# Optimization experiments

Measured on AMD Instinct MI355X. Metric: run time of the kernel, lower is better.

Reference implementation:

```python
import jax, jax.numpy as jnp
import numpy as np

B, T, I, H, O = 8192, 1024, 7, 100, 1


def setup_inputs() -> dict:
    key = jax.random.key(0)
    ks = jax.random.split(key, 7)
    s = 1.0 / np.sqrt(H)  # PyTorch default init bound for RNN/Linear(H)
    return {
        "x": jax.random.normal(ks[0], (B, T, I), dtype=jnp.float32),
        "W_ih": jax.random.uniform(ks[1], (H, I), jnp.float32, -s, s),
        "W_hh": jax.random.uniform(ks[2], (H, H), jnp.float32, -s, s),
        "b_ih": jax.random.uniform(ks[3], (H,), jnp.float32, -s, s),
        "b_hh": jax.random.uniform(ks[4], (H,), jnp.float32, -s, s),
        "W_fc": jax.random.uniform(ks[5], (O, H), jnp.float32, -s, s),
        "b_fc": jax.random.uniform(ks[6], (O,), jnp.float32, -s, s),
    }


def reference(x, W_ih, W_hh, b_ih, b_hh, W_fc, b_fc):
    # Precompute the input projection for all timesteps in one GEMM:
    # x_proj[b,t,h] = x[b,t,:] @ W_ih^T + b_ih + b_hh  (both biases folded in)
    x_proj = jnp.einsum('bti,hi->bth', x, W_ih) + b_ih + b_hh  # [B,T,H]

    def step(h, xt):
        # h_t = relu(x_t W_ih^T + b_ih + h_{t-1} W_hh^T + b_hh)
        h_new = jax.nn.relu(xt + h @ W_hh.T)
        return h_new, None

    h0 = jnp.zeros((x.shape[0], W_hh.shape[0]), dtype=x.dtype)  # [B,H]
    hT, _ = jax.lax.scan(step, h0, jnp.swapaxes(x_proj, 0, 1))  # scan over T

    # fc applied to last timestep only: out[:, -1, :] @ W_fc^T + b_fc
    return hT @ W_fc.T + b_fc  # [B,O]
```

## Files before the change

### kernel.cpp

```cpp
#include <hip/hip_runtime.h>


typedef _Float16 half8 __attribute__((ext_vector_type(8)));
typedef float f32x4 __attribute__((ext_vector_type(4)));
typedef unsigned u32x4 __attribute__((ext_vector_type(4)));

static __device__ __forceinline__ unsigned pkrtz(float a, float b) {
    return __builtin_bit_cast(unsigned, __builtin_amdgcn_cvt_pkrtz(a, b));
}

__global__ __launch_bounds__(64, 1)
void rnn_wave(const float* __restrict__ x,
              const float* __restrict__ W_ih,
              const float* __restrict__ W_hh,
              const float* __restrict__ b_ih,
              const float* __restrict__ b_hh,
              const float* __restrict__ W_fc,
              const float* __restrict__ b_fc,
              float* __restrict__ out) {
    const int l  = threadIdx.x;
    const int lm = l & 15;
    const int q  = l >> 4;
    const bool q1   = (q == 1);
    const bool qlt2 = (q < 2);

    half8 w[7][4];
#pragma unroll
    for (int ti = 0; ti < 7; ++ti) {
        const int np = 16 * ti + lm;
#pragma unroll
        for (int kt = 0; kt < 4; ++kt) {
            half8 hw;
#pragma unroll
            for (int jj = 0; jj < 8; ++jj) {
                float v = 0.f;
                if (np < 100) {
                    if (jj < 4) {
                        int p = 16 * kt + 4 * q + jj;
                        if (p < 100) v = W_hh[np * 100 + p];
                    } else if (kt < 3) {
                        int p = 16 * (kt + 4) + 4 * q + (jj - 4);
                        if (p < 100) v = W_hh[np * 100 + p];
                    } else {
                        if (q == 0)      v = W_ih[np * 7 + (jj - 4)];
                        else if (q == 1) v = (jj < 7) ? W_ih[np * 7 + jj]
                                             : (b_ih[np] + b_hh[np]);
                    }
                }
                hw[jj] = (_Float16)v;
            }
            w[ti][kt] = hw;
        }
    }

    const float* xr = x + (size_t)(blockIdx.x * 16 + lm) * 7168;
    const int o0 = q1 ? 4 : 0, o1 = o0 + 1, o2 = o0 + 2, o3 = q1 ? 6 : 3;

    half8 hf[4];
    {
        float v0 = xr[o0], v1 = xr[o1], v2 = xr[o2], v3 = xr[o3];
        u32x4 z = {0u, 0u, 0u, 0u};
        hf[0] = __builtin_bit_cast(half8, z);
        hf[1] = hf[0];
        hf[2] = hf[0];
        unsigned xd0 = pkrtz(v0, v1);
        unsigned xd1 = pkrtz(v2, q1 ? 1.0f : v3);
        if (!qlt2) { xd0 = 0u; xd1 = 0u; }
        u32x4 h3 = {0u, 0u, xd0, xd1};
        hf[3] = __builtin_bit_cast(half8, h3);
    }

    float xv[4][4];
#pragma unroll
    for (int s = 1; s <= 4; ++s) {
        const float* p = xr + s * 7;
        xv[s & 3][0] = p[o0]; xv[s & 3][1] = p[o1];
        xv[s & 3][2] = p[o2]; xv[s & 3][3] = p[o3];
    }

    const f32x4 kZ = {0.f, 0.f, 0.f, 0.f};
    f32x4 acc[7];

    for (int tb = 0; tb < 1024; tb += 4) {
#pragma unroll
        for (int u = 0; u < 4; ++u) {
            const int t = tb + u;

#pragma unroll
            for (int kt = 0; kt < 4; ++kt) {
                const int order[7] = {0, 4, 1, 5, 2, 6, 3};
#pragma unroll
                for (int oi = 0; oi < 7; ++oi) {
                    const int ti = order[oi];
                    acc[ti] = __builtin_amdgcn_mfma_f32_16x16x32_f16(
                        w[ti][kt], hf[kt], (kt == 0) ? kZ : acc[ti], 0, 0, 0);
                }
            }

            const int s = (u + 1) & 3;
#pragma unroll
            for (int kt = 0; kt < 3; ++kt) {
                u32x4 d;
                d.x = pkrtz(fmaxf(acc[kt][0], 0.f),     fmaxf(acc[kt][1], 0.f));
                d.y = pkrtz(fmaxf(acc[kt][2], 0.f),     fmaxf(acc[kt][3], 0.f));
                d.z = pkrtz(fmaxf(acc[kt + 4][0], 0.f), fmaxf(acc[kt + 4][1], 0.f));
                d.w = pkrtz(fmaxf(acc[kt + 4][2], 0.f), fmaxf(acc[kt + 4][3], 0.f));
                hf[kt] = __builtin_bit_cast(half8, d);
            }
            {
                unsigned xd0 = pkrtz(xv[s][0], xv[s][1]);
                unsigned xd1 = pkrtz(xv[s][2], q1 ? 1.0f : xv[s][3]);
                if (!qlt2) { xd0 = 0u; xd1 = 0u; }
                u32x4 d;
                d.x = pkrtz(fmaxf(acc[3][0], 0.f), fmaxf(acc[3][1], 0.f));
                d.y = pkrtz(fmaxf(acc[3][2], 0.f), fmaxf(acc[3][3], 0.f));
                d.z = xd0; d.w = xd1;
                hf[3] = __builtin_bit_cast(half8, d);
            }

            int tn = t + 5; if (tn > 1023) tn = 1023;
            const float* p = xr + tn * 7;
            xv[s][0] = p[o0]; xv[s][1] = p[o1];
            xv[s][2] = p[o2]; xv[s][3] = p[o3];
        }
    }

    float sum = 0.f;
#pragma unroll
    for (int ti = 0; ti < 7; ++ti) {
#pragma unroll
        for (int r = 0; r < 4; ++r) {
            const int np = 16 * ti + 4 * q + r;
            const float wf = (np < 100) ? W_fc[np] : 0.f;
            sum += wf * fmaxf(acc[ti][r], 0.f);
        }
    }
    sum += __shfl_xor(sum, 16, 64);
    sum += __shfl_xor(sum, 32, 64);
    if (q == 0) out[blockIdx.x * 16 + lm] = sum + b_fc[0];
}

extern "C" void kernel_launch(void* const* d_in, const int* in_sizes, int n_in,
                              void* d_out, int out_size, void* d_ws, size_t ws_size,
                              hipStream_t stream) {
    const float* x    = (const float*)d_in[0];
    const float* W_ih = (const float*)d_in[1];
    const float* W_hh = (const float*)d_in[2];
    const float* b_ih = (const float*)d_in[3];
    const float* b_hh = (const float*)d_in[4];
    const float* W_fc = (const float*)d_in[5];
    const float* b_fc = (const float*)d_in[6];
    float* out = (float*)d_out;

    rnn_wave<<<dim3(512), dim3(64), 0, stream>>>(x, W_ih, W_hh, b_ih, b_hh, W_fc, b_fc, out);
}
```

Baseline: 619.2 us.

## Interleave two independent batch tiles per wave to hide MFMA dependency latency

Each wave now processes two 16-row batch tiles (A and B) in lockstep, with interleaved MFMA chains sharing the same register-resident weights. The grid is halved to 256 blocks. This aims to fill the MFMA pipeline with independent work, since a single tile's serial recurrence leaves it stalled on dependency latency. ReLU is applied as a packed half max after conversion rather than as an fp32 fmaxf, and x loads are predicated to the lanes that need them. The trade-off is fewer waves across the CUs, on a device that has more CUs than the old 512 blocks, plus higher register pressure.

```diff
diff --git a/kernel.cpp b/kernel.cpp
--- a/kernel.cpp
+++ b/kernel.cpp
@@ -53,33 +53,43 @@
         }
     }
 
-    const float* xr = x + (size_t)(blockIdx.x * 16 + lm) * 7168;
+    const float* xrA = x + (size_t)(blockIdx.x * 32 + lm) * 7168;
+    const float* xrB = xrA + (size_t)16 * 7168;
     const int o0 = q1 ? 4 : 0, o1 = o0 + 1, o2 = o0 + 2, o3 = q1 ? 6 : 3;
 
-    half8 hf[4];
+    const u32x4 zz = {0u, 0u, 0u, 0u};
+    const half8 hz = __builtin_bit_cast(half8, zz);
+
+    half8 hfA[4], hfB[4];
     {
-        float v0 = xr[o0], v1 = xr[o1], v2 = xr[o2], v3 = xr[o3];
-        u32x4 z = {0u, 0u, 0u, 0u};
-        hf[0] = __builtin_bit_cast(half8, z);
-        hf[1] = hf[0];
-        hf[2] = hf[0];
-        unsigned xd0 = pkrtz(v0, v1);
-        unsigned xd1 = pkrtz(v2, q1 ? 1.0f : v3);
-        if (!qlt2) { xd0 = 0u; xd1 = 0u; }
-        u32x4 h3 = {0u, 0u, xd0, xd1};
-        hf[3] = __builtin_bit_cast(half8, h3);
+        float a0 = xrA[o0], a1 = xrA[o1], a2 = xrA[o2], a3 = xrA[o3];
+        float c0 = xrB[o0], c1 = xrB[o1], c2 = xrB[o2], c3 = xrB[o3];
+        hfA[0] = hz; hfA[1] = hz; hfA[2] = hz;
+        hfB[0] = hz; hfB[1] = hz; hfB[2] = hz;
+        unsigned ad0 = pkrtz(a0, a1), ad1 = pkrtz(a2, q1 ? 1.0f : a3);
+        unsigned bd0 = pkrtz(c0, c1), bd1 = pkrtz(c2, q1 ? 1.0f : c3);
+        if (!qlt2) { ad0 = 0u; ad1 = 0u; bd0 = 0u; bd1 = 0u; }
+        u32x4 ha = {0u, 0u, ad0, ad1};
+        u32x4 hb = {0u, 0u, bd0, bd1};
+        hfA[3] = __builtin_bit_cast(half8, ha);
+        hfB[3] = __builtin_bit_cast(half8, hb);
     }
 
-    float xv[4][4];
+    float xvA[4][4], xvB[4][4];
+    if (qlt2) {
 #pragma unroll
-    for (int s = 1; s <= 4; ++s) {
-        const float* p = xr + s * 7;
-        xv[s & 3][0] = p[o0]; xv[s & 3][1] = p[o1];
-        xv[s & 3][2] = p[o2]; xv[s & 3][3] = p[o3];
+        for (int s = 1; s <= 4; ++s) {
+            const float* pA = xrA + s * 7;
+            xvA[s & 3][0] = pA[o0]; xvA[s & 3][1] = pA[o1];
+            xvA[s & 3][2] = pA[o2]; xvA[s & 3][3] = pA[o3];
+            const float* pB = xrB + s * 7;
+            xvB[s & 3][0] = pB[o0]; xvB[s & 3][1] = pB[o1];
+            xvB[s & 3][2] = pB[o2]; xvB[s & 3][3] = pB[o3];
+        }
     }
 
     const f32x4 kZ = {0.f, 0.f, 0.f, 0.f};
-    f32x4 acc[7];
+    f32x4 accA[7], accB[7];
 
     for (int tb = 0; tb < 1024; tb += 4) {
 #pragma unroll
@@ -92,52 +102,76 @@
 #pragma unroll
                 for (int oi = 0; oi < 7; ++oi) {
                     const int ti = order[oi];
-                    acc[ti] = __builtin_amdgcn_mfma_f32_16x16x32_f16(
-                        w[ti][kt], hf[kt], (kt == 0) ? kZ : acc[ti], 0, 0, 0);
+                    accA[ti] = __builtin_amdgcn_mfma_f32_16x16x32_f16(
+                        w[ti][kt], hfA[kt], (kt == 0) ? kZ : accA[ti], 0, 0, 0);
+                    accB[ti] = __builtin_amdgcn_mfma_f32_16x16x32_f16(
+                        w[ti][kt], hfB[kt], (kt == 0) ? kZ : accB[ti], 0, 0, 0);
                 }
             }
 
             const int s = (u + 1) & 3;
 #pragma unroll
             for (int kt = 0; kt < 3; ++kt) {
-                u32x4 d;
-                d.x = pkrtz(fmaxf(acc[kt][0], 0.f),     fmaxf(acc[kt][1], 0.f));
-                d.y = pkrtz(fmaxf(acc[kt][2], 0.f),     fmaxf(acc[kt][3], 0.f));
-                d.z = pkrtz(fmaxf(acc[kt + 4][0], 0.f), fmaxf(acc[kt + 4][1], 0.f));
-                d.w = pkrtz(fmaxf(acc[kt + 4][2], 0.f), fmaxf(acc[kt + 4][3], 0.f));
-                hf[kt] = __builtin_bit_cast(half8, d);
+                u32x4 da, db;
+                da.x = pkrtz(accA[kt][0],     accA[kt][1]);
+                da.y = pkrtz(accA[kt][2],     accA[kt][3]);
+                da.z = pkrtz(accA[kt + 4][0], accA[kt + 4][1]);
+                da.w = pkrtz(accA[kt + 4][2], accA[kt + 4][3]);
+                hfA[kt] = __builtin_elementwise_max(__builtin_bit_cast(half8, da), hz);
+                db.x = pkrtz(accB[kt][0],     accB[kt][1]);
+                db.y = pkrtz(accB[kt][2],     accB[kt][3]);
+                db.z = pkrtz(accB[kt + 4][0], accB[kt + 4][1]);
+                db.w = pkrtz(accB[kt + 4][2], accB[kt + 4][3]);
+                hfB[kt] = __builtin_elementwise_max(__builtin_bit_cast(half8, db), hz);
             }
             {
-                unsigned xd0 = pkrtz(xv[s][0], xv[s][1]);
-                unsigned xd1 = pkrtz(xv[s][2], q1 ? 1.0f : xv[s][3]);
-                if (!qlt2) { xd0 = 0u; xd1 = 0u; }
-                u32x4 d;
-                d.x = pkrtz(fmaxf(acc[3][0], 0.f), fmaxf(acc[3][1], 0.f));
-                d.y = pkrtz(fmaxf(acc[3][2], 0.f), fmaxf(acc[3][3], 0.f));
-                d.z = xd0; d.w = xd1;
-                hf[3] = __builtin_bit_cast(half8, d);
+                unsigned ad0 = pkrtz(xvA[s][0], xvA[s][1]);
+                unsigned ad1 = pkrtz(xvA[s][2], q1 ? 1.0f : xvA[s][3]);
+                unsigned bd0 = pkrtz(xvB[s][0], xvB[s][1]);
+                unsigned bd1 = pkrtz(xvB[s][2], q1 ? 1.0f : xvB[s][3]);
+                if (!qlt2) { ad0 = 0u; ad1 = 0u; bd0 = 0u; bd1 = 0u; }
+                u32x4 da, db;
+                da.x = pkrtz(fmaxf(accA[3][0], 0.f), fmaxf(accA[3][1], 0.f));
+                da.y = pkrtz(fmaxf(accA[3][2], 0.f), fmaxf(accA[3][3], 0.f));
+                da.z = ad0; da.w = ad1;
+                db.x = pkrtz(fmaxf(accB[3][0], 0.f), fmaxf(accB[3][1], 0.f));
+                db.y = pkrtz(fmaxf(accB[3][2], 0.f), fmaxf(accB[3][3], 0.f));
+                db.z = bd0; db.w = bd1;
+                hfA[3] = __builtin_bit_cast(half8, da);
+                hfB[3] = __builtin_bit_cast(half8, db);
             }
 
             int tn = t + 5; if (tn > 1023) tn = 1023;
-            const float* p = xr + tn * 7;
-            xv[s][0] = p[o0]; xv[s][1] = p[o1];
-            xv[s][2] = p[o2]; xv[s][3] = p[o3];
+            if (qlt2) {
+                const float* pA = xrA + tn * 7;
+                xvA[s][0] = pA[o0]; xvA[s][1] = pA[o1];
+                xvA[s][2] = pA[o2]; xvA[s][3] = pA[o3];
+                const float* pB = xrB + tn * 7;
+                xvB[s][0] = pB[o0]; xvB[s][1] = pB[o1];
+                xvB[s][2] = pB[o2]; xvB[s][3] = pB[o3];
+            }
         }
     }
 
-    float sum = 0.f;
+    float sumA = 0.f, sumB = 0.f;
 #pragma unroll
     for (int ti = 0; ti < 7; ++ti) {
 #pragma unroll
         for (int r = 0; r < 4; ++r) {
             const int np = 16 * ti + 4 * q + r;
             const float wf = (np < 100) ? W_fc[np] : 0.f;
-            sum += wf * fmaxf(acc[ti][r], 0.f);
+            sumA += wf * fmaxf(accA[ti][r], 0.f);
+            sumB += wf * fmaxf(accB[ti][r], 0.f);
         }
     }
-    sum += __shfl_xor(sum, 16, 64);
-    sum += __shfl_xor(sum, 32, 64);
-    if (q == 0) out[blockIdx.x * 16 + lm] = sum + b_fc[0];
+    sumA += __shfl_xor(sumA, 16, 64);
+    sumA += __shfl_xor(sumA, 32, 64);
+    sumB += __shfl_xor(sumB, 16, 64);
+    sumB += __shfl_xor(sumB, 32, 64);
+    if (q == 0) {
+        out[blockIdx.x * 32 + lm]      = sumA + b_fc[0];
+        out[blockIdx.x * 32 + 16 + lm] = sumB + b_fc[0];
+    }
 }
 
 extern "C" void kernel_launch(void* const* d_in, const int* in_sizes, int n_in,
@@ -152,5 +186,5 @@
     const float* b_fc = (const float*)d_in[6];
     float* out = (float*)d_out;
 
-    rnn_wave<<<dim3(512), dim3(64), 0, stream>>>(x, W_ih, W_hh, b_ih, b_hh, W_fc, b_fc, out);
+    rnn_wave<<<dim3(256), dim3(64), 0, stream>>>(x, W_ih, W_hh, b_ih, b_hh, W_fc, b_fc, out);
 }
```

New measurement: 885.5 us. +43.0%, slower.
